# Kernel optimization log

Hardware: AMD Instinct MI355X
Metric: run time of the kernel (lower is better)

Reference implementation:

```python
import jax, jax.numpy as jnp
import numpy as np

N, E, G, D, L = 20000, 320000, 256, 256, 5
EPS = 1e-5


def _bn(h, g, b):
    # BatchNorm1d in training mode: biased batch statistics over the row dim
    m = h.mean(axis=0)
    v = jnp.mean((h - m) ** 2, axis=0)
    return g * (h - m) / jnp.sqrt(v + EPS) + b


def setup_inputs() -> dict:
    key = jax.random.key(0)
    ks = iter(jax.random.split(key, 40))

    def rn(shape, s=0.1):
        return jax.random.normal(next(ks), shape, dtype=jnp.float32) * s

    inp = {}
    inp['x_feats'] = jax.random.randint(next(ks), (N, 6), 0, 4)
    inp['edge_index'] = jax.random.randint(next(ks), (2, E), 0, N)
    inp['edge_attr'] = jax.random.randint(next(ks), (E, 5), 0, 2)
    inp['batch'] = jnp.sort(jax.random.randint(next(ks), (N,), 0, G))
    inp['nt1'] = rn((119, D)); inp['nt2'] = rn((4, D)); inp['nt3'] = rn((7, D))
    inp['nt4'] = rn((8, D)); inp['nt5'] = rn((5, D)); inp['nt6'] = rn((7, D))
    inp['et1'] = rn((L, 5, D)); inp['et2'] = rn((L, 4, D)); inp['et3'] = rn((L, 2, D))
    inp['et4'] = rn((L, 2, D)); inp['et5'] = rn((L, 2, D))
    inp['w1'] = rn((L, 2 * D, D)); inp['b1'] = rn((L, 2 * D))
    inp['w2'] = rn((L, D, 2 * D)); inp['b2'] = rn((L, D))
    inp['bng'] = 1.0 + rn((L, D)); inp['bnb'] = rn((L, D))
    inp['pw'] = rn((3, D, D)); inp['pg'] = 1.0 + rn((3, D)); inp['pb'] = rn((3, D))
    inp['ow1'] = rn((D // 2, D)); inp['ob1'] = rn((D // 2,))
    inp['ow2'] = rn((2, D // 2)); inp['ob2'] = rn((2,))
    return inp


def reference(x_feats, edge_index, edge_attr, batch,
              nt1, nt2, nt3, nt4, nt5, nt6,
              et1, et2, et3, et4, et5,
              w1, b1, w2, b2, bng, bnb,
              pw, pg, pb, ow1, ob1, ow2, ob2):
    n = x_feats.shape[0]
    # atom embedding: sum of 6 feature embeddings -> [N, D]
    h = (nt1[x_feats[:, 0]] + nt2[x_feats[:, 1]] + nt3[x_feats[:, 2]]
         + nt4[x_feats[:, 3]] + nt5[x_feats[:, 4]] + nt6[x_feats[:, 5]])
    src, dst = edge_index[0], edge_index[1]
    for l in range(L):
        # edge embedding for real edges: [E, D]
        e = (et1[l][edge_attr[:, 0]] + et2[l][edge_attr[:, 1]] + et3[l][edge_attr[:, 2]]
             + et4[l][edge_attr[:, 3]] + et5[l][edge_attr[:, 4]])
        # self-loop edges carry attr [4,0,0,0,0]
        self_e = et1[l][4] + et2[l][0] + et3[l][0] + et4[l][0] + et5[l][0]
        # message = x_j + e, scatter-add into destinations; self loops add h + self_e
        aggr = jax.ops.segment_sum(h[src] + e, dst, num_segments=n) + h + self_e
        # GIN MLP update: D -> 2D -> D
        hh = jax.nn.relu(aggr @ w1[l].T + b1[l]) @ w2[l].T + b2[l]
        # batchnorm then relu (dropout=0; the layer==num_layer branch is unreachable)
        h = jax.nn.relu(_bn(hh, bng[l], bnb[l]))
    # global mean pool over graphs
    counts = jax.ops.segment_sum(jnp.ones((n, 1), h.dtype), batch, num_segments=G)
    hg = jax.ops.segment_sum(h, batch, num_segments=G) / jnp.maximum(counts, 1.0)
    # proj head: (Linear no-bias, BN, ReLU) x2, then Linear no-bias + BN
    for i in range(3):
        hg = _bn(hg @ pw[i].T, pg[i], pb[i])
        if i < 2:
            hg = jax.nn.relu(hg)
    # output MLP: Linear -> Softplus -> Linear
    return jax.nn.softplus(hg @ ow1.T + ob1) @ ow2.T + ob2
```

## Files before the change

kernel.cpp:

```cpp
#include <hip/hip_runtime.h>

#define DD 256
#define TWO_D 512
#define NLAYER 5
#define NGRAPH 256
#define BNEPS 1e-5f

typedef __attribute__((ext_vector_type(8))) _Float16 half8;
typedef __attribute__((ext_vector_type(4))) _Float16 half4;
typedef __attribute__((ext_vector_type(4))) float f32x4;

#define MFMA16 __builtin_amdgcn_mfma_f32_16x16x32_f16

__global__ __launch_bounds__(256) void prep_kernel(
    const int* __restrict__ xf,
    const float* __restrict__ nt1, const float* __restrict__ nt2,
    const float* __restrict__ nt3, const float* __restrict__ nt4,
    const float* __restrict__ nt5, const float* __restrict__ nt6,
    _Float16* __restrict__ h16,
    const float* __restrict__ w1, const float* __restrict__ w2,
    _Float16* __restrict__ w1f, _Float16* __restrict__ w2f,
    const float* __restrict__ et1, const float* __restrict__ et2,
    const float* __restrict__ et3, const float* __restrict__ et4,
    const float* __restrict__ et5, _Float16* __restrict__ etab,
    int* __restrict__ deg, int* __restrict__ zr, int zr_words,
    const int* __restrict__ ei, const int* __restrict__ ea,
    int* __restrict__ packed,
    int N, int E)
{
  const int t = threadIdx.x;
  const int b = blockIdx.x;
  const int B_EMB = N;
  const int B_WC  = 128;
  const int B_ET  = NLAYER * 33;
  const int B_ZR  = 96;

  if (b < B_EMB) {
    int i = b, j = t;
    int x0 = xf[i*6+0], x1 = xf[i*6+1], x2 = xf[i*6+2];
    int x3 = xf[i*6+3], x4 = xf[i*6+4], x5 = xf[i*6+5];
    float v = nt1[x0*DD+j] + nt2[x1*DD+j] + nt3[x2*DD+j]
            + nt4[x3*DD+j] + nt5[x4*DD+j] + nt6[x5*DD+j];
    h16[(size_t)i*DD + j] = (_Float16)v;
  } else if (b < B_EMB + B_WC) {
    int bid = b - B_EMB;
    int n = NLAYER * TWO_D * DD;
    for (int i = bid*256 + t; i < n; i += B_WC*256) {
      int l = i >> 17, rem = i & 131071;
      int r = rem >> 8, k = rem & 255;
      int o1 = (l<<17) + (((r>>4)<<3) + (k>>5))*512 + ((((k>>3)&3)<<4) + (r&15))*8 + (k&7);
      w1f[o1] = (_Float16)w1[i];
      int r2 = rem >> 9, k2 = rem & 511;
      int o2 = (l<<17) + (((r2>>4)<<4) + (k2>>5))*512 + ((((k2>>3)&3)<<4) + (r2&15))*8 + (k2&7);
      w2f[o2] = (_Float16)w2[i];
    }
  } else if (b < B_EMB + B_WC + B_ET) {
    int bid = b - B_EMB - B_WC;
    int l = bid / 33, c = bid % 33;
    int j = t;
    int a0 = (c==32)?4:(c&1);
    int a1 = (c==32)?0:((c>>1)&1);
    int a2 = (c==32)?0:((c>>2)&1);
    int a3 = (c==32)?0:((c>>3)&1);
    int a4 = (c==32)?0:((c>>4)&1);
    etab[((size_t)l*33 + c)*DD + j] = (_Float16)(
        et1[(l*5+a0)*DD+j] + et2[(l*4+a1)*DD+j] + et3[(l*2+a2)*DD+j]
      + et4[(l*2+a3)*DD+j] + et5[(l*2+a4)*DD+j]);
  } else if (b < B_EMB + B_WC + B_ET + B_ZR) {
    int bid = b - B_EMB - B_WC - B_ET;
    int tw = N + zr_words;
    for (int i = bid*256 + t; i < tw; i += B_ZR*256) {
      if (i < N) deg[i] = 0;
      else zr[i - N] = 0;
    }
  } else {
    int bid = b - B_EMB - B_WC - B_ET - B_ZR;
    int e = bid*256 + t;
    if (e < E) {
      int src = ei[e];
      int code = (ea[e*5+0]&1) | ((ea[e*5+1]&1)<<1) | ((ea[e*5+2]&1)<<2)
               | ((ea[e*5+3]&1)<<3) | ((ea[e*5+4]&1)<<4);
      packed[e] = src | (code << 16);
    }
  }
}

__global__ __launch_bounds__(256) void hist_kernel(
    const int* __restrict__ ei, int* __restrict__ deg, int E)
{
  int e = blockIdx.x*256 + threadIdx.x;
  if (e < E) atomicAdd(&deg[ei[E + e]], 1);
}

__global__ __launch_bounds__(1024) void scan_kernel(
    const int* __restrict__ deg, int* __restrict__ row_start,
    int* __restrict__ cursor, int N)
{
  __shared__ int sh[1024];
  int t = threadIdx.x;
  const int CH = (N + 1023) >> 10;
  int base = t * CH;
  int lim = N - base; if (lim < 0) lim = 0; if (lim > CH) lim = CH;
  int s = 0;
  for (int i = 0; i < lim; ++i) s += deg[base + i];
  sh[t] = s;
  __syncthreads();
  for (int off = 1; off < 1024; off <<= 1) {
    int x = (t >= off) ? sh[t - off] : 0;
    __syncthreads();
    sh[t] += x;
    __syncthreads();
  }
  int run = t ? sh[t-1] : 0;
  for (int i = 0; i < lim; ++i) {
    row_start[base+i] = run; cursor[base+i] = run;
    run += deg[base+i];
  }
  if (t == 1023) row_start[N] = sh[1023];
}

__global__ __launch_bounds__(256) void scatter_kernel(
    const int* __restrict__ ei, const int* __restrict__ packed,
    int* __restrict__ cursor, int* __restrict__ esort, int E)
{
  int e = blockIdx.x*256 + threadIdx.x;
  if (e >= E) return;
  int dst = ei[E + e];
  int pos = atomicAdd(&cursor[dst], 1);
  esort[pos] = packed[e];
}

template<int APPLY_BN>
__global__ __launch_bounds__(256) void aggr_kernel(
    const _Float16* __restrict__ hsrc, const _Float16* __restrict__ etab_l,
    const int* __restrict__ row_start, const int* __restrict__ esort,
    const float* __restrict__ stats_prev, const float* __restrict__ g,
    const float* __restrict__ bb, float inv_n,
    _Float16* __restrict__ aggrh, int N)
{
  __shared__ __attribute__((aligned(16))) _Float16 se[33*DD];
  for (int i = threadIdx.x; i < 33*DD/8; i += 256)
    ((int4*)se)[i] = ((const int4*)etab_l)[i];
  __syncthreads();
  const int wave = threadIdx.x >> 6, lane = threadIdx.x & 63;
  const int c4 = lane << 2;
  float sc0=1.f, sc1=1.f, sc2=1.f, sc3=1.f, sh0=0.f, sh1=0.f, sh2=0.f, sh3=0.f;
  if (APPLY_BN) {
#define MKSC(k, SC, SH) { float m_ = stats_prev[c4+k]*inv_n;                      \
    float v_ = fmaxf(stats_prev[DD+c4+k]*inv_n - m_*m_, 0.f);                     \
    SC = g[c4+k]*rsqrtf(v_+BNEPS); SH = bb[c4+k] - m_*SC; }
    MKSC(0, sc0, sh0) MKSC(1, sc1, sh1) MKSC(2, sc2, sh2) MKSC(3, sc3, sh3)
#undef MKSC
  }
  const int W0 = blockIdx.x*4 + wave, NW = gridDim.x*4;

#define BNX(h4, o0, o1, o2, o3)                                           \
  { float t0_ = (float)(h4).x, t1_ = (float)(h4).y,                       \
          t2_ = (float)(h4).z, t3_ = (float)(h4).w;                       \
    if (APPLY_BN) {                                                       \
      t0_ = fmaxf(t0_*sc0 + sh0, 0.f); t1_ = fmaxf(t1_*sc1 + sh1, 0.f);  \
      t2_ = fmaxf(t2_*sc2 + sh2, 0.f); t3_ = fmaxf(t3_*sc3 + sh3, 0.f);  \
    }                                                                     \
    o0 = t0_; o1 = t1_; o2 = t2_; o3 = t3_; }
#define ACC4(hx, ex)                                                      \
  { float bx_, by_, bz_, bw_;                                             \
    BNX(hx, bx_, by_, bz_, bw_);                                          \
    ax += bx_ + (float)(ex).x; ay += by_ + (float)(ex).y;                 \
    az += bz_ + (float)(ex).z; aw += bw_ + (float)(ex).w; }

  for (int node = W0; node < N; node += NW) {
    int p  = row_start[node];
    int pe = row_start[node+1];
    const half4 hv = *(const half4*)(hsrc + (size_t)node*DD + c4);
    const half4 sv = *(const half4*)(se + 32*DD + c4);
    float ax, ay, az, aw;
    BNX(hv, ax, ay, az, aw);
    ax += (float)sv.x; ay += (float)sv.y; az += (float)sv.z; aw += (float)sv.w;
    for (; p + 8 <= pe; p += 8) {
      int pk0 = esort[p],   pk1 = esort[p+1], pk2 = esort[p+2], pk3 = esort[p+3];
      int pk4 = esort[p+4], pk5 = esort[p+5], pk6 = esort[p+6], pk7 = esort[p+7];
      const half4 a0 = *(const half4*)(hsrc + (size_t)(pk0 & 0xffff)*DD + c4);
      const half4 a1 = *(const half4*)(hsrc + (size_t)(pk1 & 0xffff)*DD + c4);
      const half4 a2 = *(const half4*)(hsrc + (size_t)(pk2 & 0xffff)*DD + c4);
      const half4 a3 = *(const half4*)(hsrc + (size_t)(pk3 & 0xffff)*DD + c4);
      const half4 a4 = *(const half4*)(hsrc + (size_t)(pk4 & 0xffff)*DD + c4);
      const half4 a5 = *(const half4*)(hsrc + (size_t)(pk5 & 0xffff)*DD + c4);
      const half4 a6 = *(const half4*)(hsrc + (size_t)(pk6 & 0xffff)*DD + c4);
      const half4 a7 = *(const half4*)(hsrc + (size_t)(pk7 & 0xffff)*DD + c4);
      const half4 e0 = *(const half4*)(se + (pk0 >> 16)*DD + c4);
      const half4 e1 = *(const half4*)(se + (pk1 >> 16)*DD + c4);
      const half4 e2 = *(const half4*)(se + (pk2 >> 16)*DD + c4);
      const half4 e3 = *(const half4*)(se + (pk3 >> 16)*DD + c4);
      const half4 e4 = *(const half4*)(se + (pk4 >> 16)*DD + c4);
      const half4 e5 = *(const half4*)(se + (pk5 >> 16)*DD + c4);
      const half4 e6 = *(const half4*)(se + (pk6 >> 16)*DD + c4);
      const half4 e7 = *(const half4*)(se + (pk7 >> 16)*DD + c4);
      ACC4(a0, e0) ACC4(a1, e1) ACC4(a2, e2) ACC4(a3, e3)
      ACC4(a4, e4) ACC4(a5, e5) ACC4(a6, e6) ACC4(a7, e7)
    }
    for (; p + 4 <= pe; p += 4) {
      int pk0 = esort[p], pk1 = esort[p+1], pk2 = esort[p+2], pk3 = esort[p+3];
      const half4 a0 = *(const half4*)(hsrc + (size_t)(pk0 & 0xffff)*DD + c4);
      const half4 a1 = *(const half4*)(hsrc + (size_t)(pk1 & 0xffff)*DD + c4);
      const half4 a2 = *(const half4*)(hsrc + (size_t)(pk2 & 0xffff)*DD + c4);
      const half4 a3 = *(const half4*)(hsrc + (size_t)(pk3 & 0xffff)*DD + c4);
      const half4 e0 = *(const half4*)(se + (pk0 >> 16)*DD + c4);
      const half4 e1 = *(const half4*)(se + (pk1 >> 16)*DD + c4);
      const half4 e2 = *(const half4*)(se + (pk2 >> 16)*DD + c4);
      const half4 e3 = *(const half4*)(se + (pk3 >> 16)*DD + c4);
      ACC4(a0, e0) ACC4(a1, e1) ACC4(a2, e2) ACC4(a3, e3)
    }
    for (; p < pe; ++p) {
      int pk = esort[p];
      const half4 hx = *(const half4*)(hsrc + (size_t)(pk & 0xffff)*DD + c4);
      const half4 ex = *(const half4*)(se + (pk >> 16)*DD + c4);
      ACC4(hx, ex)
    }
    half4 o;
    o.x = (_Float16)ax; o.y = (_Float16)ay; o.z = (_Float16)az; o.w = (_Float16)aw;
    *(half4*)(aggrh + (size_t)node*DD + c4) = o;
  }
#undef ACC4
#undef BNX
}

__global__ __launch_bounds__(512, 3) void mlp_kernel(
    const _Float16* __restrict__ A,
    const _Float16* __restrict__ W1f,
    const float* __restrict__ b1,
    const _Float16* __restrict__ W2f,
    const float* __restrict__ b2,
    _Float16* __restrict__ O,
    float* __restrict__ stats,
    int Nreal)
{
  __shared__ __attribute__((aligned(16))) _Float16 sA[64*256];
  __shared__ __attribute__((aligned(16))) _Float16 sH[64*128];
  const int m0 = blockIdx.x << 6;
  const int t = threadIdx.x;
  const int w = t >> 6, lane = t & 63;
  const int r15 = lane & 15, quad = lane >> 4;
  const int rx = r15 & 7;

#pragma unroll
  for (int i = 0; i < 4; ++i) {
    int seg = (i << 9) + t;
    int row = seg >> 5, s = seg & 31;
    half8 v = *(const half8*)(A + (size_t)(m0 + row)*DD + (s << 3));
    *(half8*)(sA + (row << 8) + ((s ^ (row & 7)) << 3)) = v;
  }
  __syncthreads();

  f32x4 acc2[4][2] = {};
#pragma unroll 1
  for (int c = 0; c < 4; ++c) {
    f32x4 acc1[4] = {};
    const _Float16* W1b = W1f + (((c << 3) + w) << 12);
#pragma unroll
    for (int ks = 0; ks < 8; ++ks) {
      int so = (((ks << 2) + quad) ^ rx) << 3;
      half8 bf = *(const half8*)(W1b + (ks << 9) + (lane << 3));
#pragma unroll
      for (int fm = 0; fm < 4; ++fm) {
        half8 af = *(const half8*)(sA + (((fm << 4) + r15) << 8) + so);
        acc1[fm] = MFMA16(af, bf, acc1[fm], 0, 0, 0);
      }
    }
    {
      int colL = (w << 4) + r15;
      float bv = b1[(c << 7) + colL];
      int cs = colL >> 3;
#pragma unroll
      for (int fm = 0; fm < 4; ++fm)
#pragma unroll
        for (int r = 0; r < 4; ++r) {
          int row = (fm << 4) + (quad << 2) + r;
          float v = fmaxf(acc1[fm][r] + bv, 0.f);
          sH[(row << 7) + ((cs ^ (row & 7)) << 3) + (colL & 7)] = (_Float16)v;
        }
    }
    __syncthreads();
#pragma unroll
    for (int ks = 0; ks < 4; ++ks) {
      int so = (((ks << 2) + quad) ^ rx) << 3;
      half8 b0  = *(const half8*)(W2f + (((w << 1) + 0) << 13) + (((c << 2) + ks) << 9) + (lane << 3));
      half8 b1v = *(const half8*)(W2f + (((w << 1) + 1) << 13) + (((c << 2) + ks) << 9) + (lane << 3));
#pragma unroll
      for (int fm = 0; fm < 4; ++fm) {
        half8 af = *(const half8*)(sH + (((fm << 4) + r15) << 7) + so);
        acc2[fm][0] = MFMA16(af, b0,  acc2[fm][0], 0, 0, 0);
        acc2[fm][1] = MFMA16(af, b1v, acc2[fm][1], 0, 0, 0);
      }
    }
    __syncthreads();
  }

#pragma unroll
  for (int fn = 0; fn < 2; ++fn) {
    int col = (w << 5) + (fn << 4) + r15;
    float bv = b2[col];
    float s1 = 0.f, s2 = 0.f;
#pragma unroll
    for (int fm = 0; fm < 4; ++fm)
#pragma unroll
      for (int r = 0; r < 4; ++r) {
        int row = (fm << 4) + (quad << 2) + r;
        float v = acc2[fm][fn][r] + bv;
        sA[(row << 8) + (((col >> 3) ^ (row & 7)) << 3) + (col & 7)] = (_Float16)v;
        if (m0 + row < Nreal) { s1 += v; s2 += v*v; }
      }
    s1 += __shfl_xor(s1, 16); s1 += __shfl_xor(s1, 32);
    s2 += __shfl_xor(s2, 16); s2 += __shfl_xor(s2, 32);
    if (lane < 16) { atomicAdd(&stats[col], s1); atomicAdd(&stats[DD + col], s2); }
  }
  __syncthreads();
#pragma unroll
  for (int i = 0; i < 4; ++i) {
    int seg = (i << 9) + t;
    int row = seg >> 5, s = seg & 31;
    half8 v = *(const half8*)(sA + (row << 8) + ((s ^ (row & 7)) << 3));
    *(half8*)(O + (size_t)(m0 + row)*DD + (s << 3)) = v;
  }
}

__global__ __launch_bounds__(256) void pool_kernel(
    const _Float16* __restrict__ hh16, const float* __restrict__ stats_prev,
    const float* __restrict__ g, const float* __restrict__ bb, float inv_n,
    const int* __restrict__ batch,
    float* __restrict__ hgsum, int* __restrict__ hgcnt, int N)
{
  int j = threadIdx.x;
  float m = stats_prev[j]*inv_n;
  float var = fmaxf(stats_prev[DD+j]*inv_n - m*m, 0.f);
  float sc = g[j]*rsqrtf(var + BNEPS);
  float sh = bb[j] - m*sc;
  int r0 = blockIdx.x * 16;
  int cur = -1; float acc = 0.f; int run = 0;
  for (int r = 0; r < 16; ++r) {
    int row = r0 + r;
    if (row >= N) break;
    int gg = batch[row];
    if (gg != cur) {
      if (cur >= 0) {
        atomicAdd(&hgsum[(size_t)cur*DD + j], acc);
        if (j == 0) atomicAdd(&hgcnt[cur], run);
      }
      cur = gg; acc = 0.f; run = 0;
    }
    float v = (float)hh16[(size_t)row*DD + j];
    acc += fmaxf(v*sc + sh, 0.f);
    run++;
  }
  if (cur >= 0) {
    atomicAdd(&hgsum[(size_t)cur*DD + j], acc);
    if (j == 0) atomicAdd(&hgcnt[cur], run);
  }
}

template<int MODE>
__global__ __launch_bounds__(256) void proj_gemm_kernel(
    const float* __restrict__ in, const int* __restrict__ cnt,
    const float* __restrict__ pstat_prev,
    const float* __restrict__ gprev, const float* __restrict__ bprev,
    const float* __restrict__ W,
    float* __restrict__ outb, float* __restrict__ pstat)
{
  __shared__ float sA[16][17];
  __shared__ float sB[16][17];
  int tx = threadIdx.x, ty = threadIdx.y;
  int r = blockIdx.y*16 + ty;
  int c = blockIdx.x*16 + tx;
  float acc = 0.f;
  for (int k0 = 0; k0 < DD; k0 += 16) {
    int k = k0 + tx;
    float a = in[(size_t)r*DD + k];
    if (MODE == 0) {
      a /= (float)max(cnt[r], 1);
    } else {
      float m = pstat_prev[k] * (1.0f/NGRAPH);
      float var = fmaxf(pstat_prev[DD + k] * (1.0f/NGRAPH) - m*m, 0.f);
      float sc = gprev[k] * rsqrtf(var + BNEPS);
      a = fmaxf((a - m)*sc + bprev[k], 0.f);
    }
    sA[ty][tx] = a;
    sB[ty][tx] = W[(size_t)(blockIdx.x*16 + ty)*DD + k0 + tx];
    __syncthreads();
#pragma unroll
    for (int kk = 0; kk < 16; ++kk) acc += sA[ty][kk] * sB[tx][kk];
    __syncthreads();
  }
  outb[(size_t)r*DD + c] = acc;
  sA[ty][tx] = acc; sB[ty][tx] = acc*acc;
  __syncthreads();
  for (int o = 8; o > 0; o >>= 1) {
    if (ty < o) { sA[ty][tx] += sA[ty+o][tx]; sB[ty][tx] += sB[ty+o][tx]; }
    __syncthreads();
  }
  if (ty == 0) { atomicAdd(&pstat[c], sA[0][tx]); atomicAdd(&pstat[DD + c], sB[0][tx]); }
}

__global__ __launch_bounds__(128) void out_kernel(
    const float* __restrict__ t2, const float* __restrict__ pstat2,
    const float* __restrict__ g2, const float* __restrict__ b2p,
    const float* __restrict__ ow1, const float* __restrict__ ob1,
    const float* __restrict__ ow2, const float* __restrict__ ob2,
    float* __restrict__ outp)
{
  __shared__ float rowv[DD];
  __shared__ float z[128];
  int r = blockIdx.x, t = threadIdx.x;
#pragma unroll
  for (int half = 0; half < 2; ++half) {
    int j = t + half*128;
    float m = pstat2[j] * (1.0f/NGRAPH);
    float var = fmaxf(pstat2[DD + j] * (1.0f/NGRAPH) - m*m, 0.f);
    float sc = g2[j] * rsqrtf(var + BNEPS);
    rowv[j] = (t2[(size_t)r*DD + j] - m)*sc + b2p[j];
  }
  __syncthreads();
  float a = ob1[t];
  for (int k = 0; k < DD; ++k) a += rowv[k] * ow1[(size_t)t*DD + k];
  z[t] = fmaxf(a, 0.f) + log1pf(expf(-fabsf(a)));
  __syncthreads();
  if (t < 2) {
    float o = ob2[t];
    for (int k = 0; k < 128; ++k) o += z[k] * ow2[t*128 + k];
    outp[r*2 + t] = o;
  }
}

extern "C" void kernel_launch(void* const* d_in, const int* in_sizes, int n_in,
                              void* d_out, int out_size, void* d_ws, size_t ws_size,
                              hipStream_t stream)
{
  const int* x_feats = (const int*)d_in[0];
  const int* ei      = (const int*)d_in[1];
  const int* ea      = (const int*)d_in[2];
  const int* batch   = (const int*)d_in[3];
  const float* nt1 = (const float*)d_in[4];
  const float* nt2 = (const float*)d_in[5];
  const float* nt3 = (const float*)d_in[6];
  const float* nt4 = (const float*)d_in[7];
  const float* nt5 = (const float*)d_in[8];
  const float* nt6 = (const float*)d_in[9];
  const float* et1 = (const float*)d_in[10];
  const float* et2 = (const float*)d_in[11];
  const float* et3 = (const float*)d_in[12];
  const float* et4 = (const float*)d_in[13];
  const float* et5 = (const float*)d_in[14];
  const float* w1  = (const float*)d_in[15];
  const float* b1  = (const float*)d_in[16];
  const float* w2  = (const float*)d_in[17];
  const float* b2  = (const float*)d_in[18];
  const float* bng = (const float*)d_in[19];
  const float* bnb = (const float*)d_in[20];
  const float* pw  = (const float*)d_in[21];
  const float* pg  = (const float*)d_in[22];
  const float* pb  = (const float*)d_in[23];
  const float* ow1 = (const float*)d_in[24];
  const float* ob1 = (const float*)d_in[25];
  const float* ow2 = (const float*)d_in[26];
  const float* ob2 = (const float*)d_in[27];

  const int N = in_sizes[0] / 6;
  const int E = in_sizes[1] / 2;
  const int Mp = ((N + 63) >> 6) << 6;

  unsigned char* wp = (unsigned char*)d_ws;
  size_t off = 0;
  auto carve = [&](size_t bytes) -> void* {
    void* p = wp + off;
    off += (bytes + 255) & ~(size_t)255;
    return p;
  };

  _Float16* h16      = (_Float16*)carve((size_t)N * DD * 2);
  _Float16* aggrh    = (_Float16*)carve((size_t)Mp * DD * 2);
  _Float16* hh16     = (_Float16*)carve((size_t)Mp * DD * 2);
  _Float16* w1f      = (_Float16*)carve((size_t)NLAYER * TWO_D * DD * 2);
  _Float16* w2f      = (_Float16*)carve((size_t)NLAYER * TWO_D * DD * 2);
  _Float16* etabg    = (_Float16*)carve((size_t)NLAYER * 33 * DD * 2);
  int* deg           = (int*)carve((size_t)N * 4);
  int* row_start     = (int*)carve((size_t)(N + 1) * 4);
  int* cursor        = (int*)carve((size_t)N * 4);
  int* packed        = (int*)carve((size_t)E * 4);
  int* esort         = (int*)carve((size_t)E * 4);
  float* stats       = (float*)carve((size_t)NLAYER * 2 * DD * 4);
  float* hgsum       = (float*)carve((size_t)NGRAPH * DD * 4);
  int* hgcnt         = (int*)carve((size_t)NGRAPH * 4);
  float* pstats      = (float*)carve(3 * 2 * DD * 4);
  const int ZR_WORDS = NLAYER*2*DD + NGRAPH*DD + NGRAPH + 3*2*DD;
  float* hgA         = (float*)carve((size_t)NGRAPH * DD * 4);
  float* hgB         = (float*)carve((size_t)NGRAPH * DD * 4);
  float* t0c         = (float*)carve((size_t)NGRAPH * DD * 4);
  (void)ws_size; (void)n_in; (void)out_size;

  const int EB = (E + 255) / 256;
  const float inv_n = 1.0f / (float)N;

  const int PREP_BLOCKS = N + 128 + NLAYER*33 + 96 + EB;
  prep_kernel<<<PREP_BLOCKS, 256, 0, stream>>>(
      x_feats, nt1, nt2, nt3, nt4, nt5, nt6, h16,
      w1, w2, w1f, w2f,
      et1, et2, et3, et4, et5, etabg,
      deg, (int*)stats, ZR_WORDS,
      ei, ea, packed, N, E);
  hist_kernel<<<EB, 256, 0, stream>>>(ei, deg, E);
  scan_kernel<<<1, 1024, 0, stream>>>(deg, row_start, cursor, N);
  scatter_kernel<<<EB, 256, 0, stream>>>(ei, packed, cursor, esort, E);

  const int MB = Mp >> 6;
  for (int l = 0; l < NLAYER; ++l) {
    float* st_prev = stats + (size_t)(l-1)*2*DD;
    float* st_cur  = stats + (size_t)l*2*DD;
    if (l == 0) {
      aggr_kernel<0><<<2048, 256, 0, stream>>>(h16, etabg, row_start, esort,
                                               nullptr, nullptr, nullptr, inv_n,
                                               aggrh, N);
    } else {
      aggr_kernel<1><<<2048, 256, 0, stream>>>(hh16, etabg + (size_t)l*33*DD,
                                               row_start, esort,
                                               st_prev, bng + (l-1)*DD, bnb + (l-1)*DD,
                                               inv_n, aggrh, N);
    }
    mlp_kernel<<<MB, 512, 0, stream>>>(
        aggrh, w1f + ((size_t)l << 17), b1 + l*TWO_D,
        w2f + ((size_t)l << 17), b2 + l*DD,
        hh16, st_cur, N);
  }

  pool_kernel<<<(N + 15) / 16, 256, 0, stream>>>(
      hh16, stats + (size_t)(NLAYER-1)*2*DD, bng + (NLAYER-1)*DD, bnb + (NLAYER-1)*DD,
      inv_n, batch, hgsum, hgcnt, N);

  dim3 pgrid(16, 16), pblk(16, 16);
  proj_gemm_kernel<0><<<pgrid, pblk, 0, stream>>>(
      hgsum, hgcnt, nullptr, nullptr, nullptr,
      pw + 0*DD*DD, hgA, pstats + 0*2*DD);
  proj_gemm_kernel<1><<<pgrid, pblk, 0, stream>>>(
      hgA, nullptr, pstats + 0*2*DD, pg + 0*DD, pb + 0*DD,
      pw + 1*DD*DD, hgB, pstats + 1*2*DD);
  proj_gemm_kernel<1><<<pgrid, pblk, 0, stream>>>(
      hgB, nullptr, pstats + 1*2*DD, pg + 1*DD, pb + 1*DD,
      pw + 2*DD*DD, t0c, pstats + 2*2*DD);
  out_kernel<<<NGRAPH, 128, 0, stream>>>(
      t0c, pstats + 2*2*DD, pg + 2*DD, pb + 2*DD,
      ow1, ob1, ow2, ob2, (float*)d_out);
}
```

Measured before the change: 566.1 us.

## Fuse per-layer aggregation and MLP into one kernel with a grid barrier

```diff
diff --git a/kernel.cpp b/kernel.cpp
--- a/kernel.cpp
+++ b/kernel.cpp
@@ -23,7 +23,7 @@
     const float* __restrict__ et1, const float* __restrict__ et2,
     const float* __restrict__ et3, const float* __restrict__ et4,
     const float* __restrict__ et5, _Float16* __restrict__ etab,
-    int* __restrict__ deg, int* __restrict__ zr, int zr_words,
+    int* __restrict__ deg,
     const int* __restrict__ ei, const int* __restrict__ ea,
     int* __restrict__ packed,
     int N, int E)
@@ -33,7 +33,6 @@
   const int B_EMB = N;
   const int B_WC  = 128;
   const int B_ET  = NLAYER * 33;
-  const int B_ZR  = 96;
 
   if (b < B_EMB) {
     int i = b, j = t;
@@ -66,30 +65,18 @@
     etab[((size_t)l*33 + c)*DD + j] = (_Float16)(
         et1[(l*5+a0)*DD+j] + et2[(l*4+a1)*DD+j] + et3[(l*2+a2)*DD+j]
       + et4[(l*2+a3)*DD+j] + et5[(l*2+a4)*DD+j]);
-  } else if (b < B_EMB + B_WC + B_ET + B_ZR) {
+  } else {
     int bid = b - B_EMB - B_WC - B_ET;
-    int tw = N + zr_words;
-    for (int i = bid*256 + t; i < tw; i += B_ZR*256) {
-      if (i < N) deg[i] = 0;
-      else zr[i - N] = 0;
-    }
-  } else {
-    int bid = b - B_EMB - B_WC - B_ET - B_ZR;
     int e = bid*256 + t;
     if (e < E) {
       int src = ei[e];
+      int dst = ei[E + e];
       int code = (ea[e*5+0]&1) | ((ea[e*5+1]&1)<<1) | ((ea[e*5+2]&1)<<2)
                | ((ea[e*5+3]&1)<<3) | ((ea[e*5+4]&1)<<4);
       packed[e] = src | (code << 16);
-    }
-  }
-}
-
-__global__ __launch_bounds__(256) void hist_kernel(
-    const int* __restrict__ ei, int* __restrict__ deg, int E)
-{
-  int e = blockIdx.x*256 + threadIdx.x;
-  if (e < E) atomicAdd(&deg[ei[E + e]], 1);
+      atomicAdd(&deg[dst], 1);
+    }
+  }
 }
 
 __global__ __launch_bounds__(1024) void scan_kernel(
@@ -130,123 +117,141 @@
   esort[pos] = packed[e];
 }
 
+__device__ __forceinline__ void grid_barrier(unsigned* __restrict__ bar, int nblocks)
+{
+  __threadfence();
+  __syncthreads();
+  if (threadIdx.x == 0) {
+    unsigned v = __hip_atomic_fetch_add(bar, 1u, __ATOMIC_ACQ_REL, __HIP_MEMORY_SCOPE_AGENT);
+    if (v == (unsigned)(nblocks - 1)) {
+      __hip_atomic_store(bar + 1, 1u, __ATOMIC_RELEASE, __HIP_MEMORY_SCOPE_AGENT);
+    } else {
+      while (__hip_atomic_load(bar + 1, __ATOMIC_ACQUIRE, __HIP_MEMORY_SCOPE_AGENT) == 0u) {
+        __builtin_amdgcn_s_sleep(8);
+      }
+    }
+  }
+  __syncthreads();
+  __threadfence();
+}
+
 template<int APPLY_BN>
-__global__ __launch_bounds__(256) void aggr_kernel(
+__global__ __launch_bounds__(512, 4) void layer_kernel(
     const _Float16* __restrict__ hsrc, const _Float16* __restrict__ etab_l,
     const int* __restrict__ row_start, const int* __restrict__ esort,
     const float* __restrict__ stats_prev, const float* __restrict__ g,
     const float* __restrict__ bb, float inv_n,
-    _Float16* __restrict__ aggrh, int N)
-{
-  __shared__ __attribute__((aligned(16))) _Float16 se[33*DD];
-  for (int i = threadIdx.x; i < 33*DD/8; i += 256)
-    ((int4*)se)[i] = ((const int4*)etab_l)[i];
-  __syncthreads();
-  const int wave = threadIdx.x >> 6, lane = threadIdx.x & 63;
-  const int c4 = lane << 2;
-  float sc0=1.f, sc1=1.f, sc2=1.f, sc3=1.f, sh0=0.f, sh1=0.f, sh2=0.f, sh3=0.f;
-  if (APPLY_BN) {
+    _Float16* __restrict__ aggrh,
+    const _Float16* __restrict__ W1f, const float* __restrict__ b1,
+    const _Float16* __restrict__ W2f, const float* __restrict__ b2,
+    _Float16* __restrict__ O, float* __restrict__ stats,
+    int N, int Mtiles, unsigned* __restrict__ bar)
+{
+  __shared__ __attribute__((aligned(16))) _Float16 smem[64*256 + 64*128];
+  const int t = threadIdx.x;
+  const int wave = t >> 6, lane = t & 63;
+  const int r15 = lane & 15, quad = lane >> 4;
+
+  {
+    _Float16* se = smem;
+    for (int i = t; i < 33*DD/8; i += 512)
+      ((int4*)se)[i] = ((const int4*)etab_l)[i];
+    __syncthreads();
+    const int c4 = lane << 2;
+    float sc0=1.f, sc1=1.f, sc2=1.f, sc3=1.f, sh0=0.f, sh1=0.f, sh2=0.f, sh3=0.f;
+    if (APPLY_BN) {
 #define MKSC(k, SC, SH) { float m_ = stats_prev[c4+k]*inv_n;                      \
-    float v_ = fmaxf(stats_prev[DD+c4+k]*inv_n - m_*m_, 0.f);                     \
-    SC = g[c4+k]*rsqrtf(v_+BNEPS); SH = bb[c4+k] - m_*SC; }
-    MKSC(0, sc0, sh0) MKSC(1, sc1, sh1) MKSC(2, sc2, sh2) MKSC(3, sc3, sh3)
+      float v_ = fmaxf(stats_prev[DD+c4+k]*inv_n - m_*m_, 0.f);                   \
+      SC = g[c4+k]*rsqrtf(v_+BNEPS); SH = bb[c4+k] - m_*SC; }
+      MKSC(0, sc0, sh0) MKSC(1, sc1, sh1) MKSC(2, sc2, sh2) MKSC(3, sc3, sh3)
 #undef MKSC
-  }
-  const int W0 = blockIdx.x*4 + wave, NW = gridDim.x*4;
+    }
+    const int W0 = blockIdx.x*8 + wave, NW = gridDim.x*8;
 
 #define BNX(h4, o0, o1, o2, o3)                                           \
-  { float t0_ = (float)(h4).x, t1_ = (float)(h4).y,                       \
-          t2_ = (float)(h4).z, t3_ = (float)(h4).w;                       \
-    if (APPLY_BN) {                                                       \
-      t0_ = fmaxf(t0_*sc0 + sh0, 0.f); t1_ = fmaxf(t1_*sc1 + sh1, 0.f);  \
-      t2_ = fmaxf(t2_*sc2 + sh2, 0.f); t3_ = fmaxf(t3_*sc3 + sh3, 0.f);  \
-    }                                                                     \
-    o0 = t0_; o1 = t1_; o2 = t2_; o3 = t3_; }
+    { float t0_ = (float)(h4).x, t1_ = (float)(h4).y,                     \
+            t2_ = (float)(h4).z, t3_ = (float)(h4).w;                     \
+      if (APPLY_BN) {                                                     \
+        t0_ = fmaxf(t0_*sc0 + sh0, 0.f); t1_ = fmaxf(t1_*sc1 + sh1, 0.f);\
+        t2_ = fmaxf(t2_*sc2 + sh2, 0.f); t3_ = fmaxf(t3_*sc3 + sh3, 0.f);\
+      }                                                                   \
+      o0 = t0_; o1 = t1_; o2 = t2_; o3 = t3_; }
 #define ACC4(hx, ex)                                                      \
-  { float bx_, by_, bz_, bw_;                                             \
-    BNX(hx, bx_, by_, bz_, bw_);                                          \
-    ax += bx_ + (float)(ex).x; ay += by_ + (float)(ex).y;                 \
-    az += bz_ + (float)(ex).z; aw += bw_ + (float)(ex).w; }
-
-  for (int node = W0; node < N; node += NW) {
-    int p  = row_start[node];
-    int pe = row_start[node+1];
-    const half4 hv = *(const half4*)(hsrc + (size_t)node*DD + c4);
-    const half4 sv = *(const half4*)(se + 32*DD + c4);
-    float ax, ay, az, aw;
-    BNX(hv, ax, ay, az, aw);
-    ax += (float)sv.x; ay += (float)sv.y; az += (float)sv.z; aw += (float)sv.w;
-    for (; p + 8 <= pe; p += 8) {
-      int pk0 = esort[p],   pk1 = esort[p+1], pk2 = esort[p+2], pk3 = esort[p+3];
-      int pk4 = esort[p+4], pk5 = esort[p+5], pk6 = esort[p+6], pk7 = esort[p+7];
-      const half4 a0 = *(const half4*)(hsrc + (size_t)(pk0 & 0xffff)*DD + c4);
-      const half4 a1 = *(const half4*)(hsrc + (size_t)(pk1 & 0xffff)*DD + c4);
-      const half4 a2 = *(const half4*)(hsrc + (size_t)(pk2 & 0xffff)*DD + c4);
-      const half4 a3 = *(const half4*)(hsrc + (size_t)(pk3 & 0xffff)*DD + c4);
-      const half4 a4 = *(const half4*)(hsrc + (size_t)(pk4 & 0xffff)*DD + c4);
-      const half4 a5 = *(const half4*)(hsrc + (size_t)(pk5 & 0xffff)*DD + c4);
-      const half4 a6 = *(const half4*)(hsrc + (size_t)(pk6 & 0xffff)*DD + c4);
-      const half4 a7 = *(const half4*)(hsrc + (size_t)(pk7 & 0xffff)*DD + c4);
-      const half4 e0 = *(const half4*)(se + (pk0 >> 16)*DD + c4);
-      const half4 e1 = *(const half4*)(se + (pk1 >> 16)*DD + c4);
-      const half4 e2 = *(const half4*)(se + (pk2 >> 16)*DD + c4);
-      const half4 e3 = *(const half4*)(se + (pk3 >> 16)*DD + c4);
-      const half4 e4 = *(const half4*)(se + (pk4 >> 16)*DD + c4);
-      const half4 e5 = *(const half4*)(se + (pk5 >> 16)*DD + c4);
-      const half4 e6 = *(const half4*)(se + (pk6 >> 16)*DD + c4);
-      const half4 e7 = *(const half4*)(se + (pk7 >> 16)*DD + c4);
-      ACC4(a0, e0) ACC4(a1, e1) ACC4(a2, e2) ACC4(a3, e3)
-      ACC4(a4, e4) ACC4(a5, e5) ACC4(a6, e6) ACC4(a7, e7)
-    }
-    for (; p + 4 <= pe; p += 4) {
-      int pk0 = esort[p], pk1 = esort[p+1], pk2 = esort[p+2], pk3 = esort[p+3];
-      const half4 a0 = *(const half4*)(hsrc + (size_t)(pk0 & 0xffff)*DD + c4);
-      const half4 a1 = *(const half4*)(hsrc + (size_t)(pk1 & 0xffff)*DD + c4);
-      const half4 a2 = *(const half4*)(hsrc + (size_t)(pk2 & 0xffff)*DD + c4);
-      const half4 a3 = *(const half4*)(hsrc + (size_t)(pk3 & 0xffff)*DD + c4);
-      const half4 e0 = *(const half4*)(se + (pk0 >> 16)*DD + c4);
-      const half4 e1 = *(const half4*)(se + (pk1 >> 16)*DD + c4);
-      const half4 e2 = *(const half4*)(se + (pk2 >> 16)*DD + c4);
-      const half4 e3 = *(const half4*)(se + (pk3 >> 16)*DD + c4);
-      ACC4(a0, e0) ACC4(a1, e1) ACC4(a2, e2) ACC4(a3, e3)
-    }
-    for (; p < pe; ++p) {
-      int pk = esort[p];
-      const half4 hx = *(const half4*)(hsrc + (size_t)(pk & 0xffff)*DD + c4);
-      const half4 ex = *(const half4*)(se + (pk >> 16)*DD + c4);
-      ACC4(hx, ex)
-    }
-    half4 o;
-    o.x = (_Float16)ax; o.y = (_Float16)ay; o.z = (_Float16)az; o.w = (_Float16)aw;
-    *(half4*)(aggrh + (size_t)node*DD + c4) = o;
-  }
+    { float bx_, by_, bz_, bw_;                                           \
+      BNX(hx, bx_, by_, bz_, bw_);                                        \
+      ax += bx_ + (float)(ex).x; ay += by_ + (float)(ex).y;               \
+      az += bz_ + (float)(ex).z; aw += bw_ + (float)(ex).w; }
+
+    for (int node = W0; node < N; node += NW) {
+      int p  = row_start[node];
+      int pe = row_start[node+1];
+      const half4 hv = *(const half4*)(hsrc + (size_t)node*DD + c4);
+      const half4 sv = *(const half4*)(se + 32*DD + c4);
+      float ax, ay, az, aw;
+      BNX(hv, ax, ay, az, aw);
+      ax += (float)sv.x; ay += (float)sv.y; az += (float)sv.z; aw += (float)sv.w;
+      for (; p + 8 <= pe; p += 8) {
+        int pk0 = esort[p],   pk1 = esort[p+1], pk2 = esort[p+2], pk3 = esort[p+3];
+        int pk4 = esort[p+4], pk5 = esort[p+5], pk6 = esort[p+6], pk7 = esort[p+7];
+        const half4 a0 = *(const half4*)(hsrc + (size_t)(pk0 & 0xffff)*DD + c4);
+        const half4 a1 = *(const half4*)(hsrc + (size_t)(pk1 & 0xffff)*DD + c4);
+        const half4 a2 = *(const half4*)(hsrc + (size_t)(pk2 & 0xffff)*DD + c4);
+        const half4 a3 = *(const half4*)(hsrc + (size_t)(pk3 & 0xffff)*DD + c4);
+        const half4 a4 = *(const half4*)(hsrc + (size_t)(pk4 & 0xffff)*DD + c4);
+        const half4 a5 = *(const half4*)(hsrc + (size_t)(pk5 & 0xffff)*DD + c4);
+        const half4 a6 = *(const half4*)(hsrc + (size_t)(pk6 & 0xffff)*DD + c4);
+        const half4 a7 = *(const half4*)(hsrc + (size_t)(pk7 & 0xffff)*DD + c4);
+        const half4 e0 = *(const half4*)(se + (pk0 >> 16)*DD + c4);
+        const half4 e1 = *(const half4*)(se + (pk1 >> 16)*DD + c4);
+        const half4 e2 = *(const half4*)(se + (pk2 >> 16)*DD + c4);
+        const half4 e3 = *(const half4*)(se + (pk3 >> 16)*DD + c4);
+        const half4 e4 = *(const half4*)(se + (pk4 >> 16)*DD + c4);
+        const half4 e5 = *(const half4*)(se + (pk5 >> 16)*DD + c4);
+        const half4 e6 = *(const half4*)(se + (pk6 >> 16)*DD + c4);
+        const half4 e7 = *(const half4*)(se + (pk7 >> 16)*DD + c4);
+        ACC4(a0, e0) ACC4(a1, e1) ACC4(a2, e2) ACC4(a3, e3)
+        ACC4(a4, e4) ACC4(a5, e5) ACC4(a6, e6) ACC4(a7, e7)
+      }
+      for (; p + 4 <= pe; p += 4) {
+        int pk0 = esort[p], pk1 = esort[p+1], pk2 = esort[p+2], pk3 = esort[p+3];
+        const half4 a0 = *(const half4*)(hsrc + (size_t)(pk0 & 0xffff)*DD + c4);
+        const half4 a1 = *(const half4*)(hsrc + (size_t)(pk1 & 0xffff)*DD + c4);
+        const half4 a2 = *(const half4*)(hsrc + (size_t)(pk2 & 0xffff)*DD + c4);
+        const half4 a3 = *(const half4*)(hsrc + (size_t)(pk3 & 0xffff)*DD + c4);
+        const half4 e0 = *(const half4*)(se + (pk0 >> 16)*DD + c4);
+        const half4 e1 = *(const half4*)(se + (pk1 >> 16)*DD + c4);
+        const half4 e2 = *(const half4*)(se + (pk2 >> 16)*DD + c4);
+        const half4 e3 = *(const half4*)(se + (pk3 >> 16)*DD + c4);
+        ACC4(a0, e0) ACC4(a1, e1) ACC4(a2, e2) ACC4(a3, e3)
+      }
+      for (; p < pe; ++p) {
+        int pk = esort[p];
+        const half4 hx = *(const half4*)(hsrc + (size_t)(pk & 0xffff)*DD + c4);
+        const half4 ex = *(const half4*)(se + (pk >> 16)*DD + c4);
+        ACC4(hx, ex)
+      }
+      half4 o;
+      o.x = (_Float16)ax; o.y = (_Float16)ay; o.z = (_Float16)az; o.w = (_Float16)aw;
+      *(half4*)(aggrh + (size_t)node*DD + c4) = o;
+    }
 #undef ACC4
 #undef BNX
-}
-
-__global__ __launch_bounds__(512, 3) void mlp_kernel(
-    const _Float16* __restrict__ A,
-    const _Float16* __restrict__ W1f,
-    const float* __restrict__ b1,
-    const _Float16* __restrict__ W2f,
-    const float* __restrict__ b2,
-    _Float16* __restrict__ O,
-    float* __restrict__ stats,
-    int Nreal)
-{
-  __shared__ __attribute__((aligned(16))) _Float16 sA[64*256];
-  __shared__ __attribute__((aligned(16))) _Float16 sH[64*128];
+  }
+
+  grid_barrier(bar, gridDim.x);
+
+  if (blockIdx.x >= Mtiles) return;
+  _Float16* sA = smem;
+  _Float16* sH = smem + 64*256;
   const int m0 = blockIdx.x << 6;
-  const int t = threadIdx.x;
-  const int w = t >> 6, lane = t & 63;
-  const int r15 = lane & 15, quad = lane >> 4;
+  const int w = wave;
   const int rx = r15 & 7;
 
 #pragma unroll
   for (int i = 0; i < 4; ++i) {
     int seg = (i << 9) + t;
     int row = seg >> 5, s = seg & 31;
-    half8 v = *(const half8*)(A + (size_t)(m0 + row)*DD + (s << 3));
+    half8 v = *(const half8*)(aggrh + (size_t)(m0 + row)*DD + (s << 3));
     *(half8*)(sA + (row << 8) + ((s ^ (row & 7)) << 3)) = v;
   }
   __syncthreads();
@@ -307,7 +312,7 @@
         int row = (fm << 4) + (quad << 2) + r;
         float v = acc2[fm][fn][r] + bv;
         sA[(row << 8) + (((col >> 3) ^ (row & 7)) << 3) + (col & 7)] = (_Float16)v;
-        if (m0 + row < Nreal) { s1 += v; s2 += v*v; }
+        if (m0 + row < N) { s1 += v; s2 += v*v; }
       }
     s1 += __shfl_xor(s1, 16); s1 += __shfl_xor(s1, 32);
     s2 += __shfl_xor(s2, 16); s2 += __shfl_xor(s2, 32);
@@ -489,7 +494,8 @@
   float* hgsum       = (float*)carve((size_t)NGRAPH * DD * 4);
   int* hgcnt         = (int*)carve((size_t)NGRAPH * 4);
   float* pstats      = (float*)carve(3 * 2 * DD * 4);
-  const int ZR_WORDS = NLAYER*2*DD + NGRAPH*DD + NGRAPH + 3*2*DD;
+  unsigned* bar      = (unsigned*)carve(256);
+  const size_t ZR_BYTES = 10240 + 262144 + 1024 + 6144 + 256;
   float* hgA         = (float*)carve((size_t)NGRAPH * DD * 4);
   float* hgB         = (float*)carve((size_t)NGRAPH * DD * 4);
   float* t0c         = (float*)carve((size_t)NGRAPH * DD * 4);
@@ -498,35 +504,37 @@
   const int EB = (E + 255) / 256;
   const float inv_n = 1.0f / (float)N;
 
-  const int PREP_BLOCKS = N + 128 + NLAYER*33 + 96 + EB;
+  hipMemsetAsync(deg, 0, (size_t)N * 4, stream);
+  hipMemsetAsync(stats, 0, ZR_BYTES, stream);
+
+  const int PREP_BLOCKS = N + 128 + NLAYER*33 + EB;
   prep_kernel<<<PREP_BLOCKS, 256, 0, stream>>>(
       x_feats, nt1, nt2, nt3, nt4, nt5, nt6, h16,
       w1, w2, w1f, w2f,
       et1, et2, et3, et4, et5, etabg,
-      deg, (int*)stats, ZR_WORDS,
-      ei, ea, packed, N, E);
-  hist_kernel<<<EB, 256, 0, stream>>>(ei, deg, E);
+      deg, ei, ea, packed, N, E);
   scan_kernel<<<1, 1024, 0, stream>>>(deg, row_start, cursor, N);
   scatter_kernel<<<EB, 256, 0, stream>>>(ei, packed, cursor, esort, E);
 
-  const int MB = Mp >> 6;
+  const int Mtiles = Mp >> 6;
+  const int LGRID = 512;
   for (int l = 0; l < NLAYER; ++l) {
     float* st_prev = stats + (size_t)(l-1)*2*DD;
     float* st_cur  = stats + (size_t)l*2*DD;
     if (l == 0) {
-      aggr_kernel<0><<<2048, 256, 0, stream>>>(h16, etabg, row_start, esort,
-                                               nullptr, nullptr, nullptr, inv_n,
-                                               aggrh, N);
+      layer_kernel<0><<<LGRID, 512, 0, stream>>>(
+          h16, etabg, row_start, esort,
+          nullptr, nullptr, nullptr, inv_n, aggrh,
+          w1f, b1, w2f, b2,
+          hh16, st_cur, N, Mtiles, bar + 2*l);
     } else {
-      aggr_kernel<1><<<2048, 256, 0, stream>>>(hh16, etabg + (size_t)l*33*DD,
-                                               row_start, esort,
-                                               st_prev, bng + (l-1)*DD, bnb + (l-1)*DD,
-                                               inv_n, aggrh, N);
-    }
-    mlp_kernel<<<MB, 512, 0, stream>>>(
-        aggrh, w1f + ((size_t)l << 17), b1 + l*TWO_D,
-        w2f + ((size_t)l << 17), b2 + l*DD,
-        hh16, st_cur, N);
+      layer_kernel<1><<<LGRID, 512, 0, stream>>>(
+          hh16, etabg + (size_t)l*33*DD, row_start, esort,
+          st_prev, bng + (l-1)*DD, bnb + (l-1)*DD, inv_n, aggrh,
+          w1f + ((size_t)l << 17), b1 + l*TWO_D,
+          w2f + ((size_t)l << 17), b2 + l*DD,
+          hh16, st_cur, N, Mtiles, bar + 2*l);
+    }
   }
 
   pool_kernel<<<(N + 15) / 16, 256, 0, stream>>>(
```

After: 1.658 ms. +192.8%, slower.
